# Performance work log

Hardware: AMD Instinct MI355X
Metric: run time of the kernel (lower is better)

The kernel has to match this reference:

```python
import jax, jax.numpy as jnp
import numpy as np

B, T, D = 2048, 200, 64
H1, H2 = 128, 64
NEG_INF = jnp.float32(-(2.0**32) + 1.0)


def setup_inputs() -> dict:
    key = jax.random.key(0)
    ks = jax.random.split(key, 10)
    query = jax.random.normal(ks[0], (B, D), dtype=jnp.float32)
    k = jax.random.normal(ks[1], (B, T, D), dtype=jnp.float32)
    v = jax.random.normal(ks[2], (B, T, D), dtype=jnp.float32)
    mask = jax.random.randint(ks[3], (B, T), 0, 2, dtype=jnp.int32)
    # Deep_layer params: concat width 4*D -> H1 -> H2 -> 1
    s1 = 1.0 / np.sqrt(4 * D)
    s2 = 1.0 / np.sqrt(H1)
    s3 = 1.0 / np.sqrt(H2)
    W1 = jax.random.normal(ks[4], (4 * D, H1), dtype=jnp.float32) * s1
    b1 = jnp.zeros((H1,), dtype=jnp.float32)
    W2 = jax.random.normal(ks[5], (H1, H2), dtype=jnp.float32) * s2
    b2 = jnp.zeros((H2,), dtype=jnp.float32)
    Wo = jax.random.normal(ks[6], (H2, 1), dtype=jnp.float32) * s3
    bo = jnp.zeros((1,), dtype=jnp.float32)
    return {"query": query, "key": k, "value": v, "mask": mask,
            "W1": W1, "b1": b1, "W2": W2, "b2": b2, "Wo": Wo, "bo": bo}


def reference(query, key, value, mask, W1, b1, W2, b2, Wo, bo):
    b, t, d = key.shape
    q = jnp.broadcast_to(query[:, None, :], (b, t, d))          # tile query over T
    emb = jnp.concatenate([q, key, q - key, q * key], axis=-1)  # [B,T,4D]
    h = jax.nn.relu(jnp.einsum('btf,fh->bth', emb, W1) + b1)    # [B,T,H1]
    h = jax.nn.relu(jnp.einsum('bth,hk->btk', h, W2) + b2)      # [B,T,H2]
    score = (jnp.einsum('btk,ko->bto', h, Wo) + bo)[..., 0]     # [B,T]
    score = jnp.where(mask == 0, NEG_INF, score)
    attn = jax.nn.softmax(score, axis=-1)                       # [B,T]
    out = jnp.einsum('bt,btd->bd', attn, value)                 # [B,D]
    return out
```

## Files before the change

kernel.cpp:

```cpp
#include <hip/hip_runtime.h>
#include <hip/hip_bf16.h>
#include <cstdint>
#include <cstddef>

#define NB 2048
#define NT 200
#define ND 64
#define NH1 128
#define NH2 64
#define NTILES 7
#define NTP 224

typedef __bf16 bf16x8 __attribute__((ext_vector_type(8)));
typedef float f32x4 __attribute__((ext_vector_type(4)));

#define MFMA16(A, Bv, C) __builtin_amdgcn_mfma_f32_16x16x32_bf16((A), (Bv), (C), 0, 0, 0)

union BF8u { __bf16 b[8]; bf16x8 v; uint4 u4; };
union BF4u { __bf16 b[4]; uint2 u2; };

template<int N>
__device__ __forceinline__ float row_ror_add(float v) {
    int r = __builtin_amdgcn_update_dpp(0, __builtin_bit_cast(int, v),
                                        0x120 | N, 0xF, 0xF, false);
    return v + __builtin_bit_cast(float, r);
}

__device__ __forceinline__ void bar_sync() {
    __builtin_amdgcn_sched_barrier(0);
    asm volatile("s_waitcnt lgkmcnt(0)" ::: "memory");
    __builtin_amdgcn_s_barrier();
    __builtin_amdgcn_sched_barrier(0);
}

__global__ void prep_kernel(const float* __restrict__ W1, const float* __restrict__ W2,
                            float* __restrict__ Qp, float* __restrict__ AbT,
                            float* __restrict__ PT, __bf16* __restrict__ W2t) {
    int tid = blockIdx.x * blockDim.x + threadIdx.x;
    if (tid < 64 * NH1) {
        int c = tid >> 7, j = tid & 127;
        Qp[tid] = W1[c * NH1 + j] + W1[(128 + c) * NH1 + j];
        int jj = tid >> 6, cc = tid & 63;
        AbT[tid] = W1[(64 + cc) * NH1 + jj] - W1[(128 + cc) * NH1 + jj];
        PT[tid]  = W1[(192 + cc) * NH1 + jj];
        int j2 = tid >> 7, k = tid & 127;
        W2t[tid] = (__bf16)W2[k * NH2 + j2];
    }
}

__global__ __launch_bounds__(256, 4)
void attn_main(const float* __restrict__ query, const float* __restrict__ key,
               const float* __restrict__ value, const int* __restrict__ mask,
               const float* __restrict__ b1, const float* __restrict__ b2,
               const float* __restrict__ Wo,
               const float* __restrict__ Qp, const float* __restrict__ AbT,
               const float* __restrict__ PT, const __bf16* __restrict__ W2t,
               float* __restrict__ out)
{
    __shared__ __align__(16) char smem[30976];
    auto KHI0 = (__bf16(*)[72])(smem);
    auto KHI1 = (__bf16(*)[72])(smem + 4608);
    auto H10  = (__bf16(*)[136])(smem + 9216);
    auto H11  = (__bf16(*)[136])(smem + 17920);
    auto SP   = (float(*)[NTP])(smem + 26624);
    float* QS  = (float*)(smem + 30208);
    float* QHS = (float*)(smem + 30464);
    float* SCORES = (float*)(smem);
    auto REDS = (float(*)[72])(smem + 9216);

    const int b = blockIdx.x;
    const int tid = threadIdx.x;
    const int lane = tid & 63;
    const int wave = tid >> 6;
    const int jn = lane & 15;
    const int g4 = lane >> 4;
    const int g8 = g4 * 8;

    const int r_st = tid >> 3;
    const int c0   = (tid & 7) * 8;
    const float* kp_base = key + (size_t)b * NT * ND + c0;
    float4 pf[2][2];

    {
        const float* kp0 = kp_base + (size_t)r_st * ND;
        pf[0][0] = *(const float4*)(kp0);
        pf[0][1] = *(const float4*)(kp0 + 4);
        const float* kp1 = kp_base + (size_t)(32 + r_st) * ND;
        pf[1][0] = *(const float4*)(kp1);
        pf[1][1] = *(const float4*)(kp1 + 4);
    }

    if (tid < ND) QS[tid] = query[(size_t)b * ND + tid];
    int mk = 0;
    if (tid < NT) mk = mask[(size_t)b * NT + tid];
    bar_sync();

    if (tid < NH1) {
        float a0 = 0.f, a1 = 0.f, a2 = 0.f, a3 = 0.f;
        #pragma unroll
        for (int c = 0; c < ND; c += 4) {
            a0 = fmaf(QS[c],     Qp[c * NH1 + tid],       a0);
            a1 = fmaf(QS[c + 1], Qp[(c + 1) * NH1 + tid], a1);
            a2 = fmaf(QS[c + 2], Qp[(c + 2) * NH1 + tid], a2);
            a3 = fmaf(QS[c + 3], Qp[(c + 3) * NH1 + tid], a3);
        }
        QHS[tid] = b1[tid] + ((a0 + a1) + (a2 + a3));
    }

    bf16x8 g1_b[2][2];
    const int jown = wave * 32;
    #pragma unroll
    for (int n = 0; n < 2; ++n) {
        const int j = jown + n * 16 + jn;
        #pragma unroll
        for (int kk = 0; kk < 2; ++kk) {
            const float* ab = AbT + j * ND + kk * 32 + g8;
            const float* pt = PT  + j * ND + kk * 32 + g8;
            float4 a0 = *(const float4*)ab, a1 = *(const float4*)(ab + 4);
            float4 p0 = *(const float4*)pt, p1 = *(const float4*)(pt + 4);
            const float va[8] = {a0.x,a0.y,a0.z,a0.w,a1.x,a1.y,a1.z,a1.w};
            const float vp[8] = {p0.x,p0.y,p0.z,p0.w,p1.x,p1.y,p1.z,p1.w};
            BF8u vh;
            #pragma unroll
            for (int e = 0; e < 8; ++e) {
                const int c = kk * 32 + g8 + e;
                vh.b[e] = (__bf16)fmaf(QS[c], vp[e], va[e]);
            }
            g1_b[n][kk] = vh.v;
        }
    }
    bf16x8 g2_w[4];
    {
        const int j2 = wave * 16 + jn;
        #pragma unroll
        for (int kk = 0; kk < 4; ++kk)
            g2_w[kk] = *(const bf16x8*)(W2t + j2 * NH1 + kk * 32 + g8);
    }
    bar_sync();

    float qh4[2][4];
    {
        const float4 qa = *(const float4*)(QHS + jown + g4 * 4);
        const float4 qb = *(const float4*)(QHS + jown + 16 + g4 * 4);
        qh4[0][0] = qa.x; qh4[0][1] = qa.y; qh4[0][2] = qa.z; qh4[0][3] = qa.w;
        qh4[1][0] = qb.x; qh4[1][1] = qb.y; qh4[1][2] = qb.z; qh4[1][3] = qb.w;
    }
    const float b2j = b2[wave * 16 + jn];
    const float woj = Wo[wave * 16 + jn];

    f32x4 accc[2][2];
    #pragma unroll
    for (int ti = 0; ti <= NTILES; ++ti) {
        __bf16 (*KCUR)[72]   = (ti & 1) ? KHI1 : KHI0;
        __bf16 (*H1CUR)[136] = ((ti + 1) & 1) ? H11 : H10;

        if (ti < NTILES) {
            const int bi = ti & 1;
            const float vals[8] = {pf[bi][0].x, pf[bi][0].y, pf[bi][0].z, pf[bi][0].w,
                                   pf[bi][1].x, pf[bi][1].y, pf[bi][1].z, pf[bi][1].w};
            BF8u ph;
            #pragma unroll
            for (int i = 0; i < 8; ++i) ph.b[i] = (__bf16)vals[i];
            *(uint4*)(&KCUR[r_st][c0]) = ph.u4;
        }
        if (ti > 0) {
            #pragma unroll
            for (int mt = 0; mt < 2; ++mt) {
                const int trow = mt * 16 + jn;
                #pragma unroll
                for (int n = 0; n < 2; ++n) {
                    BF4u pk;
                    #pragma unroll
                    for (int r = 0; r < 4; ++r)
                        pk.b[r] = (__bf16)fmaxf(accc[mt][n][r] + qh4[n][r], 0.f);
                    *(uint2*)(&H1CUR[trow][jown + n * 16 + g4 * 4]) = pk.u2;
                }
            }
        }
        bar_sync();

        if (ti + 2 < NTILES) {
            const int bi = ti & 1;
            int t = (ti + 2) * 32 + r_st;
            t = t < NT ? t : NT - 1;
            const float* kp = kp_base + (size_t)t * ND;
            pf[bi][0] = *(const float4*)(kp);
            pf[bi][1] = *(const float4*)(kp + 4);
        }
        if (ti < NTILES) {
            #pragma unroll
            for (int mt = 0; mt < 2; ++mt) {
                const int arow = mt * 16 + jn;
                const bf16x8 k0 = *(const bf16x8*)(&KCUR[arow][g8]);
                const bf16x8 k1 = *(const bf16x8*)(&KCUR[arow][32 + g8]);
                #pragma unroll
                for (int n = 0; n < 2; ++n) {
                    f32x4 ac = {0.f, 0.f, 0.f, 0.f};
                    ac = MFMA16(g1_b[n][0], k0, ac);
                    ac = MFMA16(g1_b[n][1], k1, ac);
                    accc[mt][n] = ac;
                }
            }
        }
        if (ti > 0) {
            const int t0 = (ti - 1) * 32;
            #pragma unroll
            for (int mt = 0; mt < 2; ++mt) {
                const int arow = mt * 16 + jn;
                const bf16x8 h0v = *(const bf16x8*)(&H1CUR[arow][g8]);
                const bf16x8 h1v = *(const bf16x8*)(&H1CUR[arow][32 + g8]);
                const bf16x8 h2v = *(const bf16x8*)(&H1CUR[arow][64 + g8]);
                const bf16x8 h3v = *(const bf16x8*)(&H1CUR[arow][96 + g8]);
                f32x4 cA = {0.f,0.f,0.f,0.f}, cB = {0.f,0.f,0.f,0.f};
                cA = MFMA16(h0v, g2_w[0], cA);
                cB = MFMA16(h1v, g2_w[1], cB);
                cA = MFMA16(h2v, g2_w[2], cA);
                cB = MFMA16(h3v, g2_w[3], cB);
                #pragma unroll
                for (int r = 0; r < 4; ++r) {
                    float v = fmaxf(cA[r] + cB[r] + b2j, 0.f) * woj;
                    v = row_ror_add<8>(v);
                    v = row_ror_add<4>(v);
                    v = row_ror_add<2>(v);
                    v = row_ror_add<1>(v);
                    if (jn == 0) SP[wave][t0 + mt * 16 + g4 * 4 + r] = v;
                }
            }
        }
    }

    const int tg = tid >> 4;
    const int dq = tid & 15;
    const float* vbase = value + (size_t)b * NT * ND + dq * 4;
    const float4 vv0 = *(const float4*)(vbase + (size_t)tg * ND);
    const float4 vv1 = *(const float4*)(vbase + (size_t)(tg + 16) * ND);

    bar_sync();

    if (tid < NTP) {
        const float sc = SP[0][tid] + SP[1][tid] + SP[2][tid] + SP[3][tid];
        SCORES[tid] = (tid < NT && mk != 0) ? __expf(sc) : 0.f;
    }
    bar_sync();

    {
        const float e0 = SCORES[tg], e1 = SCORES[tg + 16];
        float oa0 = fmaf(e1, vv1.x, e0 * vv0.x);
        float oa1 = fmaf(e1, vv1.y, e0 * vv0.y);
        float oa2 = fmaf(e1, vv1.z, e0 * vv0.z);
        float oa3 = fmaf(e1, vv1.w, e0 * vv0.w);
        float den = e0 + e1;
        #pragma unroll 4
        for (int t = tg + 32; t < NT; t += 16) {
            const float e = SCORES[t];
            const float4 v4 = *(const float4*)(vbase + (size_t)t * ND);
            oa0 = fmaf(e, v4.x, oa0); oa1 = fmaf(e, v4.y, oa1);
            oa2 = fmaf(e, v4.z, oa2); oa3 = fmaf(e, v4.w, oa3);
            den += e;
        }
        REDS[tg][dq*4+0] = oa0; REDS[tg][dq*4+1] = oa1;
        REDS[tg][dq*4+2] = oa2; REDS[tg][dq*4+3] = oa3;
        if (dq == 0) REDS[tg][64] = den;
    }
    bar_sync();

    if (tid < ND) {
        float s = 0.f, den = 0.f;
        #pragma unroll
        for (int g = 0; g < 16; ++g) { s += REDS[g][tid]; den += REDS[g][64]; }
        out[(size_t)b * ND + tid] = s / den;
    }
}

extern "C" void kernel_launch(void* const* d_in, const int* in_sizes, int n_in,
                              void* d_out, int out_size, void* d_ws, size_t ws_size,
                              hipStream_t stream) {
    const float* query = (const float*)d_in[0];
    const float* key   = (const float*)d_in[1];
    const float* value = (const float*)d_in[2];
    const int*   maskp = (const int*)d_in[3];
    const float* W1    = (const float*)d_in[4];
    const float* b1    = (const float*)d_in[5];
    const float* W2    = (const float*)d_in[6];
    const float* b2    = (const float*)d_in[7];
    const float* Wo    = (const float*)d_in[8];
    float* out = (float*)d_out;

    float* Qp  = (float*)d_ws;
    float* AbT = Qp + 64 * NH1;
    float* PT  = AbT + NH1 * ND;
    __bf16* W2t = (__bf16*)(PT + NH1 * ND);

    prep_kernel<<<32, 256, 0, stream>>>(W1, W2, Qp, AbT, PT, W2t);
    attn_main<<<NB, 256, 0, stream>>>(query, key, value, maskp, b1, b2, Wo,
                                      Qp, AbT, PT, W2t, out);
}
```

Before: 54.20 us.

## Restructure tile loop into three-stage pipeline with layer-1 compute after K store

Rewrites the per-tile loop as a three-stage software pipeline: convert and store K for tile ti, compute layer-1 MFMA and write ReLU H1 for tile ti-1, and compute layer-2 MFMA and scores for tile ti-2, with a single barrier per iteration. The layer-1 accumulators are now produced and consumed within one iteration instead of living across a barrier. This aims to cut live registers and rebalance work between barriers. The cost is one extra loop iteration and one more barrier, which adds latency to the prologue and epilogue.

```diff
diff --git a/kernel.cpp b/kernel.cpp
--- a/kernel.cpp
+++ b/kernel.cpp
@@ -148,22 +148,44 @@
     const float b2j = b2[wave * 16 + jn];
     const float woj = Wo[wave * 16 + jn];
 
-    f32x4 accc[2][2];
     #pragma unroll
-    for (int ti = 0; ti <= NTILES; ++ti) {
-        __bf16 (*KCUR)[72]   = (ti & 1) ? KHI1 : KHI0;
-        __bf16 (*H1CUR)[136] = ((ti + 1) & 1) ? H11 : H10;
-
+    for (int ti = 0; ti <= NTILES + 1; ++ti) {
         if (ti < NTILES) {
+            __bf16 (*KW)[72] = (ti & 1) ? KHI1 : KHI0;
             const int bi = ti & 1;
             const float vals[8] = {pf[bi][0].x, pf[bi][0].y, pf[bi][0].z, pf[bi][0].w,
                                    pf[bi][1].x, pf[bi][1].y, pf[bi][1].z, pf[bi][1].w};
             BF8u ph;
             #pragma unroll
             for (int i = 0; i < 8; ++i) ph.b[i] = (__bf16)vals[i];
-            *(uint4*)(&KCUR[r_st][c0]) = ph.u4;
-        }
-        if (ti > 0) {
+            *(uint4*)(&KW[r_st][c0]) = ph.u4;
+        }
+        if (ti + 2 < NTILES) {
+            const int bi = ti & 1;
+            int t = (ti + 2) * 32 + r_st;
+            t = t < NT ? t : NT - 1;
+            const float* kp = kp_base + (size_t)t * ND;
+            pf[bi][0] = *(const float4*)(kp);
+            pf[bi][1] = *(const float4*)(kp + 4);
+        }
+        if (ti >= 1 && ti <= NTILES) {
+            const int tp = ti - 1;
+            __bf16 (*KR)[72]  = (tp & 1) ? KHI1 : KHI0;
+            __bf16 (*H1W)[136] = (tp & 1) ? H11 : H10;
+            f32x4 accc[2][2];
+            #pragma unroll
+            for (int mt = 0; mt < 2; ++mt) {
+                const int arow = mt * 16 + jn;
+                const bf16x8 k0 = *(const bf16x8*)(&KR[arow][g8]);
+                const bf16x8 k1 = *(const bf16x8*)(&KR[arow][32 + g8]);
+                #pragma unroll
+                for (int n = 0; n < 2; ++n) {
+                    f32x4 ac = {0.f, 0.f, 0.f, 0.f};
+                    ac = MFMA16(g1_b[n][0], k0, ac);
+                    ac = MFMA16(g1_b[n][1], k1, ac);
+                    accc[mt][n] = ac;
+                }
+            }
             #pragma unroll
             for (int mt = 0; mt < 2; ++mt) {
                 const int trow = mt * 16 + jn;
@@ -173,44 +195,21 @@
                     #pragma unroll
                     for (int r = 0; r < 4; ++r)
                         pk.b[r] = (__bf16)fmaxf(accc[mt][n][r] + qh4[n][r], 0.f);
-                    *(uint2*)(&H1CUR[trow][jown + n * 16 + g4 * 4]) = pk.u2;
+                    *(uint2*)(&H1W[trow][jown + n * 16 + g4 * 4]) = pk.u2;
                 }
             }
         }
-        bar_sync();
-
-        if (ti + 2 < NTILES) {
-            const int bi = ti & 1;
-            int t = (ti + 2) * 32 + r_st;
-            t = t < NT ? t : NT - 1;
-            const float* kp = kp_base + (size_t)t * ND;
-            pf[bi][0] = *(const float4*)(kp);
-            pf[bi][1] = *(const float4*)(kp + 4);
-        }
-        if (ti < NTILES) {
+        if (ti >= 2) {
+            const int tq = ti - 2;
+            __bf16 (*H1R)[136] = (tq & 1) ? H11 : H10;
+            const int t0 = tq * 32;
             #pragma unroll
             for (int mt = 0; mt < 2; ++mt) {
                 const int arow = mt * 16 + jn;
-                const bf16x8 k0 = *(const bf16x8*)(&KCUR[arow][g8]);
-                const bf16x8 k1 = *(const bf16x8*)(&KCUR[arow][32 + g8]);
-                #pragma unroll
-                for (int n = 0; n < 2; ++n) {
-                    f32x4 ac = {0.f, 0.f, 0.f, 0.f};
-                    ac = MFMA16(g1_b[n][0], k0, ac);
-                    ac = MFMA16(g1_b[n][1], k1, ac);
-                    accc[mt][n] = ac;
-                }
-            }
-        }
-        if (ti > 0) {
-            const int t0 = (ti - 1) * 32;
-            #pragma unroll
-            for (int mt = 0; mt < 2; ++mt) {
-                const int arow = mt * 16 + jn;
-                const bf16x8 h0v = *(const bf16x8*)(&H1CUR[arow][g8]);
-                const bf16x8 h1v = *(const bf16x8*)(&H1CUR[arow][32 + g8]);
-                const bf16x8 h2v = *(const bf16x8*)(&H1CUR[arow][64 + g8]);
-                const bf16x8 h3v = *(const bf16x8*)(&H1CUR[arow][96 + g8]);
+                const bf16x8 h0v = *(const bf16x8*)(&H1R[arow][g8]);
+                const bf16x8 h1v = *(const bf16x8*)(&H1R[arow][32 + g8]);
+                const bf16x8 h2v = *(const bf16x8*)(&H1R[arow][64 + g8]);
+                const bf16x8 h3v = *(const bf16x8*)(&H1R[arow][96 + g8]);
                 f32x4 cA = {0.f,0.f,0.f,0.f}, cB = {0.f,0.f,0.f,0.f};
                 cA = MFMA16(h0v, g2_w[0], cA);
                 cB = MFMA16(h1v, g2_w[1], cB);
@@ -227,6 +226,7 @@
                 }
             }
         }
+        if (ti <= NTILES) bar_sync();
     }
 
     const int tg = tid >> 4;
```

New measurement: 54.75 us. Within noise of the previous version (+1.0%).

## Restructure tile loop into three-stage pipeline with one barrier per stage

Applied to the files above, without the earlier changes.

Reworks the per-tile loop into a three-stage software pipeline. Each step stages K tile ti, computes layer-1 MFMA plus ReLU for tile ti-1 and writes its H1, then runs layer-2 for tile ti-2. This leaves one barrier per step instead of having layer-1 results held in registers across the barrier. The loop is now a non-unrolled loop over pairs of macro-expanded regions, and many unroll pragmas are removed, which cuts code size but may leave inner loops rolled and add a pipeline step.

```diff
diff --git a/kernel.cpp b/kernel.cpp
--- a/kernel.cpp
+++ b/kernel.cpp
@@ -97,7 +97,6 @@
 
     if (tid < NH1) {
         float a0 = 0.f, a1 = 0.f, a2 = 0.f, a3 = 0.f;
-        #pragma unroll
         for (int c = 0; c < ND; c += 4) {
             a0 = fmaf(QS[c],     Qp[c * NH1 + tid],       a0);
             a1 = fmaf(QS[c + 1], Qp[(c + 1) * NH1 + tid], a1);
@@ -109,10 +108,8 @@
 
     bf16x8 g1_b[2][2];
     const int jown = wave * 32;
-    #pragma unroll
     for (int n = 0; n < 2; ++n) {
         const int j = jown + n * 16 + jn;
-        #pragma unroll
         for (int kk = 0; kk < 2; ++kk) {
             const float* ab = AbT + j * ND + kk * 32 + g8;
             const float* pt = PT  + j * ND + kk * 32 + g8;
@@ -121,7 +118,6 @@
             const float va[8] = {a0.x,a0.y,a0.z,a0.w,a1.x,a1.y,a1.z,a1.w};
             const float vp[8] = {p0.x,p0.y,p0.z,p0.w,p1.x,p1.y,p1.z,p1.w};
             BF8u vh;
-            #pragma unroll
             for (int e = 0; e < 8; ++e) {
                 const int c = kk * 32 + g8 + e;
                 vh.b[e] = (__bf16)fmaf(QS[c], vp[e], va[e]);
@@ -132,7 +128,6 @@
     bf16x8 g2_w[4];
     {
         const int j2 = wave * 16 + jn;
-        #pragma unroll
         for (int kk = 0; kk < 4; ++kk)
             g2_w[kk] = *(const bf16x8*)(W2t + j2 * NH1 + kk * 32 + g8);
     }
@@ -148,86 +143,84 @@
     const float b2j = b2[wave * 16 + jn];
     const float woj = Wo[wave * 16 + jn];
 
-    f32x4 accc[2][2];
-    #pragma unroll
-    for (int ti = 0; ti <= NTILES; ++ti) {
-        __bf16 (*KCUR)[72]   = (ti & 1) ? KHI1 : KHI0;
-        __bf16 (*H1CUR)[136] = ((ti + 1) & 1) ? H11 : H10;
-
-        if (ti < NTILES) {
-            const int bi = ti & 1;
-            const float vals[8] = {pf[bi][0].x, pf[bi][0].y, pf[bi][0].z, pf[bi][0].w,
-                                   pf[bi][1].x, pf[bi][1].y, pf[bi][1].z, pf[bi][1].w};
-            BF8u ph;
-            #pragma unroll
-            for (int i = 0; i < 8; ++i) ph.b[i] = (__bf16)vals[i];
-            *(uint4*)(&KCUR[r_st][c0]) = ph.u4;
-        }
-        if (ti > 0) {
-            #pragma unroll
-            for (int mt = 0; mt < 2; ++mt) {
-                const int trow = mt * 16 + jn;
-                #pragma unroll
-                for (int n = 0; n < 2; ++n) {
-                    BF4u pk;
-                    #pragma unroll
-                    for (int r = 0; r < 4; ++r)
-                        pk.b[r] = (__bf16)fmaxf(accc[mt][n][r] + qh4[n][r], 0.f);
-                    *(uint2*)(&H1CUR[trow][jown + n * 16 + g4 * 4]) = pk.u2;
-                }
-            }
-        }
-        bar_sync();
-
-        if (ti + 2 < NTILES) {
-            const int bi = ti & 1;
-            int t = (ti + 2) * 32 + r_st;
-            t = t < NT ? t : NT - 1;
-            const float* kp = kp_base + (size_t)t * ND;
-            pf[bi][0] = *(const float4*)(kp);
-            pf[bi][1] = *(const float4*)(kp + 4);
-        }
-        if (ti < NTILES) {
-            #pragma unroll
-            for (int mt = 0; mt < 2; ++mt) {
-                const int arow = mt * 16 + jn;
-                const bf16x8 k0 = *(const bf16x8*)(&KCUR[arow][g8]);
-                const bf16x8 k1 = *(const bf16x8*)(&KCUR[arow][32 + g8]);
-                #pragma unroll
-                for (int n = 0; n < 2; ++n) {
-                    f32x4 ac = {0.f, 0.f, 0.f, 0.f};
-                    ac = MFMA16(g1_b[n][0], k0, ac);
-                    ac = MFMA16(g1_b[n][1], k1, ac);
-                    accc[mt][n] = ac;
-                }
-            }
-        }
-        if (ti > 0) {
-            const int t0 = (ti - 1) * 32;
-            #pragma unroll
-            for (int mt = 0; mt < 2; ++mt) {
-                const int arow = mt * 16 + jn;
-                const bf16x8 h0v = *(const bf16x8*)(&H1CUR[arow][g8]);
-                const bf16x8 h1v = *(const bf16x8*)(&H1CUR[arow][32 + g8]);
-                const bf16x8 h2v = *(const bf16x8*)(&H1CUR[arow][64 + g8]);
-                const bf16x8 h3v = *(const bf16x8*)(&H1CUR[arow][96 + g8]);
-                f32x4 cA = {0.f,0.f,0.f,0.f}, cB = {0.f,0.f,0.f,0.f};
-                cA = MFMA16(h0v, g2_w[0], cA);
-                cB = MFMA16(h1v, g2_w[1], cB);
-                cA = MFMA16(h2v, g2_w[2], cA);
-                cB = MFMA16(h3v, g2_w[3], cB);
-                #pragma unroll
-                for (int r = 0; r < 4; ++r) {
-                    float v = fmaxf(cA[r] + cB[r] + b2j, 0.f) * woj;
-                    v = row_ror_add<8>(v);
-                    v = row_ror_add<4>(v);
-                    v = row_ror_add<2>(v);
-                    v = row_ror_add<1>(v);
-                    if (jn == 0) SP[wave][t0 + mt * 16 + g4 * 4 + r] = v;
-                }
-            }
-        }
-    }
+#define REGION(TI, P)                                                          \
+    {                                                                          \
+        const int ti = (TI);                                                   \
+        if (ti < NTILES) {                            \
+            __bf16 (*KW)[72] = (P) ? KHI1 : KHI0;                              \
+            const float vals[8] = {pf[P][0].x, pf[P][0].y, pf[P][0].z,         \
+                                   pf[P][0].w, pf[P][1].x, pf[P][1].y,         \
+                                   pf[P][1].z, pf[P][1].w};                    \
+            BF8u ph;                                                           \
+            for (int i = 0; i < 8; ++i) ph.b[i] = (__bf16)vals[i];             \
+            *(uint4*)(&KW[r_st][c0]) = ph.u4;                                  \
+        }                                                                      \
+        if (ti + 2 < NTILES) {                   \
+            int t = (ti + 2) * 32 + r_st;                                      \
+            t = t < NT ? t : NT - 1;                                           \
+            const float* kp = kp_base + (size_t)t * ND;                        \
+            pf[P][0] = *(const float4*)(kp);                                   \
+            pf[P][1] = *(const float4*)(kp + 4);                               \
+        }                                                                      \
+        if (ti >= 1 && ti <= NTILES) {           \
+            __bf16 (*KR)[72]   = (P) ? KHI0 : KHI1;        \
+            __bf16 (*H1W)[136] = (P) ? H10 : H11;          \
+            f32x4 accc[2][2];                                                  \
+            for (int mt = 0; mt < 2; ++mt) {                                   \
+                const int arow = mt * 16 + jn;                                 \
+                const bf16x8 k0 = *(const bf16x8*)(&KR[arow][g8]);             \
+                const bf16x8 k1 = *(const bf16x8*)(&KR[arow][32 + g8]);        \
+                for (int n = 0; n < 2; ++n) {                                  \
+                    f32x4 ac = {0.f, 0.f, 0.f, 0.f};                           \
+                    ac = MFMA16(g1_b[n][0], k0, ac);                           \
+                    ac = MFMA16(g1_b[n][1], k1, ac);                           \
+                    accc[mt][n] = ac;                                          \
+                }                                                              \
+            }                                                                  \
+            for (int mt = 0; mt < 2; ++mt) {                                   \
+                const int trow = mt * 16 + jn;                                 \
+                for (int n = 0; n < 2; ++n) {                                  \
+                    BF4u pk;                                                   \
+                    for (int r = 0; r < 4; ++r)                                \
+                        pk.b[r] = (__bf16)fmaxf(accc[mt][n][r] + qh4[n][r],    \
+                                                0.f);                          \
+                    *(uint2*)(&H1W[trow][jown + n * 16 + g4 * 4]) = pk.u2;     \
+                }                                                              \
+            }                                                                  \
+        }                                                                      \
+        if (ti >= 2) {                          \
+            __bf16 (*H1R)[136] = (P) ? H11 : H10;            \
+            const int t0 = (ti - 2) * 32;                                      \
+            for (int mt = 0; mt < 2; ++mt) {                                   \
+                const int arow = mt * 16 + jn;                                 \
+                const bf16x8 h0v = *(const bf16x8*)(&H1R[arow][g8]);           \
+                const bf16x8 h1v = *(const bf16x8*)(&H1R[arow][32 + g8]);      \
+                const bf16x8 h2v = *(const bf16x8*)(&H1R[arow][64 + g8]);      \
+                const bf16x8 h3v = *(const bf16x8*)(&H1R[arow][96 + g8]);      \
+                f32x4 cA = {0.f,0.f,0.f,0.f}, cB = {0.f,0.f,0.f,0.f};          \
+                cA = MFMA16(h0v, g2_w[0], cA);                                 \
+                cB = MFMA16(h1v, g2_w[1], cB);                                 \
+                cA = MFMA16(h2v, g2_w[2], cA);                                 \
+                cB = MFMA16(h3v, g2_w[3], cB);                                 \
+                for (int r = 0; r < 4; ++r) {                                  \
+                    float v = fmaxf(cA[r] + cB[r] + b2j, 0.f) * woj;           \
+                    v = row_ror_add<8>(v);                                     \
+                    v = row_ror_add<4>(v);                                     \
+                    v = row_ror_add<2>(v);                                     \
+                    v = row_ror_add<1>(v);                                     \
+                    if (jn == 0) SP[wave][t0 + mt * 16 + g4 * 4 + r] = v;      \
+                }                                                              \
+            }                                                                  \
+        }                                                                      \
+        if (ti <= NTILES) bar_sync();                                          \
+    }
+
+    #pragma unroll 1
+    for (int tt = 0; tt <= NTILES + 1; tt += 2) {
+        REGION(tt, 0)
+        if (tt + 1 <= NTILES + 1) REGION(tt + 1, 1)
+    }
+#undef REGION
 
     const int tg = tid >> 4;
     const int dq = tid & 15;
@@ -266,7 +259,6 @@
 
     if (tid < ND) {
         float s = 0.f, den = 0.f;
-        #pragma unroll
         for (int g = 0; g < 16; ++g) { s += REDS[g][tid]; den += REDS[g][64]; }
         out[(size_t)b * ND + tid] = s / den;
     }
```

Result: slower. 57.48 us (+6.0%).
